# Kernel optimization log

Measured on AMD Instinct MI355X. Metric: run time of the kernel, lower is better.

The kernel has to match this reference:

```python
import jax, jax.numpy as jnp
import numpy as np

VOCAB = 50000
D = 256
NUM_GROUPS = 2
NUM_BEAMS = 4
MAX_LEN = 24
DIV_STRENGTH = 0.5


def setup_inputs() -> dict:
    key = jax.random.key(0)
    k1, k2, k3, k4 = jax.random.split(key, 4)
    B, S = 8, 128
    src = jax.random.normal(k1, (B, S, D), jnp.float32)
    We = jax.random.normal(k2, (D, D), jnp.float32) * (1.0 / np.sqrt(D))
    Emb = jax.random.normal(k3, (VOCAB, D), jnp.float32) * 0.02
    Wout = jax.random.normal(k4, (D, VOCAB), jnp.float32) * (1.0 / np.sqrt(D))
    return {"src": src, "We": We, "Emb": Emb, "Wout": Wout}


def _beam_search(src, We, Emb, Wout):
    B = src.shape[0]
    K, V, L = NUM_BEAMS, VOCAB, MAX_LEN

    # encoder: linear projection; decoder context = mean-pooled encoder output
    enc_out = jnp.einsum('bsd,de->bse', src, We)      # [B, S, D]
    ctx = enc_out.mean(axis=1)                        # [B, D]
    ctx_rep = jnp.repeat(ctx, K, axis=0)              # [B*K, D]
    beam_ids = jnp.arange(K)[:, None, None]           # [K,1,1]

    all_seqs, all_scores = [], []
    for g in range(NUM_GROUPS):
        prev = jnp.stack(all_seqs) if g > 0 else None  # [g, B, K, L]

        def step(carry, t, prev=prev):
            seqs, gs = carry                           # [B,K,L] int32, [B,K] f32
            tok = jax.lax.dynamic_index_in_dim(seqs, t - 1, axis=2, keepdims=False)  # [B,K]
            h = Emb[tok.reshape(-1)] + ctx_rep         # [B*K, D]
            logits = h @ Wout                          # [B*K, V]
            scores = jax.nn.log_softmax(logits, axis=-1).reshape(B, K, V)
            if prev is not None:
                # diversity penalty: subtract strength once per token present
                # anywhere (any batch, pos < t) in prev group's beam b (unique() semantics)
                posmask = (jnp.arange(L) < t).astype(scores.dtype)   # [L]
                w = jnp.broadcast_to(posmask, (K, B, L))

                def presence(pseq):                    # pseq: [B,K,L]
                    tok_t = pseq.transpose(1, 0, 2)    # [K,B,L]
                    cnt = jnp.zeros((K, V), scores.dtype).at[beam_ids, tok_t].add(w)
                    return (cnt > 0).astype(scores.dtype)

                pen = jax.vmap(presence)(prev).sum(axis=0)           # [K,V]
                scores = scores - DIV_STRENGTH * pen[None, :, :]
            total = (gs[:, :, None] + scores).reshape(B, K * V)
            topk_scores, topk_idx = jax.lax.top_k(total, K)          # [B,K]
            beam_idx = topk_idx // V
            next_tok = topk_idx % V
            seqs = jnp.take_along_axis(seqs, beam_idx[:, :, None], axis=1)
            seqs = seqs.at[:, :, t].set(next_tok)
            return (seqs, topk_scores), None

        init_scores = jnp.full((B, K), -1e9, jnp.float32).at[:, 0].set(0.0)
        init_seqs = jnp.zeros((B, K, L), jnp.int32).at[:, :, 0].set(1)  # BOS=1
        (seqs, gscores), _ = jax.lax.scan(step, (init_seqs, init_scores), jnp.arange(1, L))
        all_seqs.append(seqs)
        all_scores.append(gscores)

    return jnp.concatenate(all_seqs, axis=1), jnp.concatenate(all_scores, axis=1)


def reference(src, We, Emb, Wout):
    # returns (final_sequences [B, G*K, L] int32, final_scores [B, G*K] f32)
    return _beam_search(src, We, Emb, Wout)
```

## Files before the change

### kernel.cpp

```cpp
#include <hip/hip_runtime.h>
#include <math.h>

#define VOCAB 50000
#define DM 256
#define NB 8
#define NK 4
#define SL 24
#define NROW 32
#define CBLK 256
#define NXB 196
#define NPART NXB
#define DIVS 0.5f
#define NCH 49
#define SCH 1024

__device__ __forceinline__ bool cbetter(float av, int ai, float bv, int bi) {
  return (av > bv) || (av == bv && ai < bi);
}

__device__ __forceinline__ void merge4(const float* av, const int* ai,
                                       const float* bv, const int* bi,
                                       float* rv, int* ri) {
  int x = 0, y = 0;
#pragma unroll
  for (int j = 0; j < 4; ++j) {
    bool ta = cbetter(av[x], ai[x], bv[y], bi[y]);
    rv[j] = ta ? av[x] : bv[y];
    ri[j] = ta ? ai[x] : bi[y];
    if (ta) ++x; else ++y;
  }
}

__global__ void k_prep(const float* __restrict__ src, const float* __restrict__ We,
                       float* __restrict__ ctx) {
  int b = blockIdx.x, d = threadIdx.x;
  __shared__ float sm[DM];
  const float* p = src + (size_t)b * 128 * DM + d;
  float s = 0.f;
  for (int i = 0; i < 128; ++i) s += p[i * DM];
  sm[d] = s * (1.f / 128.f);
  __syncthreads();
  float acc = 0.f;
  for (int dp = 0; dp < DM; ++dp) acc += sm[dp] * We[dp * DM + d];
  ctx[b * DM + d] = acc;
}

__global__ void k_eprep(const float* __restrict__ Emb, const float* __restrict__ ctx,
                        const int* __restrict__ seq, float* __restrict__ eg, int t) {
  int r = blockIdx.x, d = threadIdx.x;
  int tok = seq[r * SL + (t - 1)];
  eg[r * DM + d] = Emb[(size_t)tok * DM + d] + ctx[(r >> 2) * DM + d];
}

__global__ void k_wtile(const float* __restrict__ Wout, float* __restrict__ WT) {
  int b = blockIdx.x, d = blockIdx.y, c = threadIdx.x;
  int col = b * CBLK + c;
  WT[(size_t)b * (CBLK * DM) + d * CBLK + c] =
      (col < VOCAB) ? Wout[(size_t)d * VOCAB + col] : 0.f;
}

__global__ __launch_bounds__(512) void k_logits_tiled(
    const float* __restrict__ WT, const float* __restrict__ eg,
    float* __restrict__ logits, float* __restrict__ pm, float* __restrict__ ps) {
  int tid = threadIdx.x;
  int lane = tid & 63, wq = tid >> 6;
  int c0 = blockIdx.x * CBLK + lane * 4;
  bool valid = (c0 + 3 < VOCAB);
  const float* wbase = WT + (size_t)blockIdx.x * (CBLK * DM) + lane * 4;
  int rb = __builtin_amdgcn_readfirstlane(wq) * 4;
  const float* e0 = eg + (size_t)rb * DM;
  float acc[4][4];
#pragma unroll
  for (int r = 0; r < 4; ++r)
#pragma unroll
    for (int c = 0; c < 4; ++c) acc[r][c] = 0.f;

  for (int d = 0; d < DM; d += 8) {
    float4 w[8];
#pragma unroll
    for (int j = 0; j < 8; ++j)
      w[j] = *reinterpret_cast<const float4*>(wbase + (size_t)(d + j) * CBLK);
#pragma unroll
    for (int r = 0; r < 4; ++r) {
      const float* ep = e0 + r * DM + d;
      const float4 ea = *reinterpret_cast<const float4*>(ep);
      const float4 eb = *reinterpret_cast<const float4*>(ep + 4);
#pragma unroll
      for (int c = 0; c < 4; ++c) {
        float a = acc[r][c];
        a = fmaf(ea.x, (&w[0].x)[c], a);
        a = fmaf(ea.y, (&w[1].x)[c], a);
        a = fmaf(ea.z, (&w[2].x)[c], a);
        a = fmaf(ea.w, (&w[3].x)[c], a);
        a = fmaf(eb.x, (&w[4].x)[c], a);
        a = fmaf(eb.y, (&w[5].x)[c], a);
        a = fmaf(eb.z, (&w[6].x)[c], a);
        a = fmaf(eb.w, (&w[7].x)[c], a);
        acc[r][c] = a;
      }
    }
  }
  if (valid) {
#pragma unroll
    for (int r = 0; r < 4; ++r) {
      float4 o = make_float4(acc[r][0], acc[r][1], acc[r][2], acc[r][3]);
      *reinterpret_cast<float4*>(&logits[(size_t)(rb + r) * VOCAB + c0]) = o;
    }
  }
#pragma unroll
  for (int r = 0; r < 4; ++r) {
    float m = valid ? fmaxf(fmaxf(acc[r][0], acc[r][1]), fmaxf(acc[r][2], acc[r][3]))
                    : -INFINITY;
#pragma unroll
    for (int o = 32; o >= 1; o >>= 1) m = fmaxf(m, __shfl_xor(m, o));
    float sv = 0.f;
    if (valid && m != -INFINITY) {
      sv = expf(acc[r][0] - m) + expf(acc[r][1] - m) +
           expf(acc[r][2] - m) + expf(acc[r][3] - m);
    }
#pragma unroll
    for (int o = 32; o >= 1; o >>= 1) sv += __shfl_xor(sv, o);
    if (lane == 0) {
      pm[(size_t)(rb + r) * NPART + blockIdx.x] = m;
      ps[(size_t)(rb + r) * NPART + blockIdx.x] = sv;
    }
  }
}

__global__ __launch_bounds__(512) void k_logits_flat(
    const float* __restrict__ Wout, const float* __restrict__ eg,
    float* __restrict__ logits, float* __restrict__ pm, float* __restrict__ ps) {
  int tid = threadIdx.x;
  int lane = tid & 63, wq = tid >> 6;
  int c0 = blockIdx.x * CBLK + lane * 4;
  bool valid = (c0 + 3 < VOCAB);
  const float* wbase = Wout + (valid ? c0 : (VOCAB - 4));
  int rb = __builtin_amdgcn_readfirstlane(wq) * 4;
  const float* e0 = eg + (size_t)rb * DM;
  float acc[4][4];
#pragma unroll
  for (int r = 0; r < 4; ++r)
#pragma unroll
    for (int c = 0; c < 4; ++c) acc[r][c] = 0.f;
  for (int d = 0; d < DM; d += 8) {
    float4 w[8];
#pragma unroll
    for (int j = 0; j < 8; ++j)
      w[j] = *reinterpret_cast<const float4*>(wbase + (size_t)(d + j) * VOCAB);
#pragma unroll
    for (int r = 0; r < 4; ++r) {
      const float* ep = e0 + r * DM + d;
      const float4 ea = *reinterpret_cast<const float4*>(ep);
      const float4 eb = *reinterpret_cast<const float4*>(ep + 4);
#pragma unroll
      for (int c = 0; c < 4; ++c) {
        float a = acc[r][c];
        a = fmaf(ea.x, (&w[0].x)[c], a);
        a = fmaf(ea.y, (&w[1].x)[c], a);
        a = fmaf(ea.z, (&w[2].x)[c], a);
        a = fmaf(ea.w, (&w[3].x)[c], a);
        a = fmaf(eb.x, (&w[4].x)[c], a);
        a = fmaf(eb.y, (&w[5].x)[c], a);
        a = fmaf(eb.z, (&w[6].x)[c], a);
        a = fmaf(eb.w, (&w[7].x)[c], a);
        acc[r][c] = a;
      }
    }
  }
  if (valid) {
#pragma unroll
    for (int r = 0; r < 4; ++r) {
      float4 o = make_float4(acc[r][0], acc[r][1], acc[r][2], acc[r][3]);
      *reinterpret_cast<float4*>(&logits[(size_t)(rb + r) * VOCAB + c0]) = o;
    }
  }
#pragma unroll
  for (int r = 0; r < 4; ++r) {
    float m = valid ? fmaxf(fmaxf(acc[r][0], acc[r][1]), fmaxf(acc[r][2], acc[r][3]))
                    : -INFINITY;
#pragma unroll
    for (int o = 32; o >= 1; o >>= 1) m = fmaxf(m, __shfl_xor(m, o));
    float sv = 0.f;
    if (valid && m != -INFINITY) {
      sv = expf(acc[r][0] - m) + expf(acc[r][1] - m) +
           expf(acc[r][2] - m) + expf(acc[r][3] - m);
    }
#pragma unroll
    for (int o = 32; o >= 1; o >>= 1) sv += __shfl_xor(sv, o);
    if (lane == 0) {
      pm[(size_t)(rb + r) * NPART + blockIdx.x] = m;
      ps[(size_t)(rb + r) * NPART + blockIdx.x] = sv;
    }
  }
}

__global__ __launch_bounds__(256) void k_topk_s1(
    const float* __restrict__ logits, const float* __restrict__ pm,
    const float* __restrict__ ps, const float* __restrict__ gs_src,
    const int* __restrict__ minpos, float* __restrict__ s1v,
    int* __restrict__ s1i, int t, int g) {
  int b = blockIdx.x / NCH, c = blockIdx.x % NCH, tid = threadIdx.x;
  int lane = tid & 63, wave = tid >> 6;
  __shared__ float gsv[NK], lsev[NK];
  __shared__ float lv[256][4];
  __shared__ int li[256][4];
  if (tid < NK) gsv[tid] = gs_src[b * NK + tid];
  {
    int row = b * NK + wave;
    const float* pmr = pm + (size_t)row * NPART;
    const float* psr = ps + (size_t)row * NPART;
    float M = -INFINITY, S = 0.f;
    for (int j = lane; j < NPART; j += 64) {
      float mj = pmr[j];
      if (mj != -INFINITY) {
        float sj = psr[j];
        float Mn = fmaxf(M, mj);
        S = (M == -INFINITY) ? sj * expf(mj - Mn)
                             : S * expf(M - Mn) + sj * expf(mj - Mn);
        M = Mn;
      }
    }
#pragma unroll
    for (int o = 32; o >= 1; o >>= 1) {
      float Mo = __shfl_xor(M, o);
      float So = __shfl_xor(S, o);
      if (Mo != -INFINITY) {
        float Mn = fmaxf(M, Mo);
        S = (M == -INFINITY) ? So * expf(Mo - Mn)
                             : S * expf(M - Mn) + So * expf(Mo - Mn);
        M = Mn;
      }
    }
    if (lane == 0) lsev[wave] = M + logf(S);
  }
  __syncthreads();

  float tv[4]; int ti[4];
#pragma unroll
  for (int j = 0; j < 4; ++j) { tv[j] = -INFINITY; ti[j] = 0x7fffffff; }

  int v = c * SCH + tid * 4;
  for (int k = 0; k < NK; ++k) {
    float gsk = gsv[k], lsek = lsev[k];
    const float* lrow = logits + (size_t)(b * NK + k) * VOCAB;
    const int* mp = minpos + (size_t)k * VOCAB;
    if (v + 3 < VOCAB) {
      float4 x4 = *reinterpret_cast<const float4*>(lrow + v);
      float xs[4] = {x4.x, x4.y, x4.z, x4.w};
      int pen[4] = {0, 0, 0, 0};
      if (g) {
        int4 m4 = *reinterpret_cast<const int4*>(mp + v);
        pen[0] = m4.x < t; pen[1] = m4.y < t; pen[2] = m4.z < t; pen[3] = m4.w < t;
      }
#pragma unroll
      for (int i = 0; i < 4; ++i) {
        float sc = xs[i] - lsek;
        if (pen[i]) sc -= DIVS;
        float x = gsk + sc;
        int idx = k * VOCAB + v + i;
        if (cbetter(x, idx, tv[3], ti[3])) {
          int pos = 3;
          if (cbetter(x, idx, tv[2], ti[2])) { tv[3]=tv[2]; ti[3]=ti[2]; pos=2;
            if (cbetter(x, idx, tv[1], ti[1])) { tv[2]=tv[1]; ti[2]=ti[1]; pos=1;
              if (cbetter(x, idx, tv[0], ti[0])) { tv[1]=tv[0]; ti[1]=ti[0]; pos=0; } } }
          tv[pos] = x; ti[pos] = idx;
        }
      }
    } else {
#pragma unroll
      for (int i = 0; i < 4; ++i) {
        int vv = v + i;
        if (vv >= VOCAB) break;
        float sc = lrow[vv] - lsek;
        if (g && mp[vv] < t) sc -= DIVS;
        float x = gsk + sc;
        int idx = k * VOCAB + vv;
        if (cbetter(x, idx, tv[3], ti[3])) {
          int pos = 3;
          if (cbetter(x, idx, tv[2], ti[2])) { tv[3]=tv[2]; ti[3]=ti[2]; pos=2;
            if (cbetter(x, idx, tv[1], ti[1])) { tv[2]=tv[1]; ti[2]=ti[1]; pos=1;
              if (cbetter(x, idx, tv[0], ti[0])) { tv[1]=tv[0]; ti[1]=ti[0]; pos=0; } } }
          tv[pos] = x; ti[pos] = idx;
        }
      }
    }
  }
#pragma unroll
  for (int j = 0; j < 4; ++j) { lv[tid][j] = tv[j]; li[tid][j] = ti[j]; }
  __syncthreads();
  for (int s = 128; s >= 1; s >>= 1) {
    if (tid < s) {
      float av[4], bv[4], rv[4]; int ai[4], bi[4], ri[4];
#pragma unroll
      for (int j = 0; j < 4; ++j) { av[j]=lv[tid][j]; ai[j]=li[tid][j]; bv[j]=lv[tid+s][j]; bi[j]=li[tid+s][j]; }
      merge4(av, ai, bv, bi, rv, ri);
#pragma unroll
      for (int j = 0; j < 4; ++j) { lv[tid][j]=rv[j]; li[tid][j]=ri[j]; }
    }
    __syncthreads();
  }
  if (tid == 0) {
#pragma unroll
    for (int j = 0; j < 4; ++j) {
      s1v[(b * NCH + c) * 4 + j] = lv[0][j];
      s1i[(b * NCH + c) * 4 + j] = li[0][j];
    }
  }
}

__global__ __launch_bounds__(256) void k_topk_s2(
    const float* __restrict__ s1v, const int* __restrict__ s1i,
    const int* __restrict__ seq_src, const float* __restrict__ Emb,
    const float* __restrict__ ctx, float* __restrict__ gs_dst,
    int* __restrict__ seq_dst, float* __restrict__ eg,
    int t, int g, float* __restrict__ out) {
  int b = blockIdx.x, tid = threadIdx.x;
  __shared__ float lv[64][4];
  __shared__ int li[64][4];
  __shared__ int oldseq[NK * SL];
  __shared__ float selv[NK];
  __shared__ int selb[NK], selt[NK];
  if (tid < 64) {
#pragma unroll
    for (int j = 0; j < 4; ++j) {
      if (tid < NCH) { lv[tid][j] = s1v[(b * NCH + tid) * 4 + j]; li[tid][j] = s1i[(b * NCH + tid) * 4 + j]; }
      else { lv[tid][j] = -INFINITY; li[tid][j] = 0x7fffffff; }
    }
  }
  if (tid < NK * SL) oldseq[tid] = seq_src[b * NK * SL + tid];
  __syncthreads();
  for (int s = 32; s >= 1; s >>= 1) {
    if (tid < s) {
      float av[4], bv[4], rv[4]; int ai[4], bi[4], ri[4];
#pragma unroll
      for (int j = 0; j < 4; ++j) { av[j]=lv[tid][j]; ai[j]=li[tid][j]; bv[j]=lv[tid+s][j]; bi[j]=li[tid+s][j]; }
      merge4(av, ai, bv, bi, rv, ri);
#pragma unroll
      for (int j = 0; j < 4; ++j) { lv[tid][j]=rv[j]; li[tid][j]=ri[j]; }
    }
    __syncthreads();
  }
  if (tid == 0) {
#pragma unroll
    for (int j = 0; j < 4; ++j) {
      selv[j] = lv[0][j];
      selb[j] = li[0][j] / VOCAB;
      selt[j] = li[0][j] % VOCAB;
    }
  }
  __syncthreads();
  if (tid < NK * SL) {
    int j = tid / SL, l = tid % SL;
    int tok = (l == t) ? selt[j] : oldseq[selb[j] * SL + l];
    seq_dst[b * NK * SL + tid] = tok;
    if (t == SL - 1) out[(size_t)b * (2 * NK * SL) + (g * NK + j) * SL + l] = (float)tok;
  }
  if (tid < NK) {
    gs_dst[b * NK + tid] = selv[tid];
    if (t == SL - 1) out[NB * 2 * NK * SL + b * (2 * NK) + g * NK + tid] = selv[tid];
  }
  if (t < SL - 1) {
    int d = tid;
#pragma unroll
    for (int j = 0; j < NK; ++j) {
      int nt_ = selt[j];
      eg[(size_t)(b * NK + j) * DM + d] = Emb[(size_t)nt_ * DM + d] + ctx[b * DM + d];
    }
  }
}

__global__ void k_init(int* __restrict__ seqA, float* __restrict__ gsA) {
  int i = threadIdx.x;
  seqA[i] = (i % SL == 0) ? 1 : 0;
  if (i < NB * NK) gsA[i] = ((i & 3) == 0) ? 0.f : -1e9f;
}

__global__ void k_minpos_init(int* __restrict__ minpos) {
  int i = blockIdx.x * 256 + threadIdx.x;
  if (i < NK * VOCAB) minpos[i] = 1 << 30;
}

__global__ void k_minpos_scatter(const int* __restrict__ seq, int* __restrict__ minpos) {
  int i = threadIdx.x;
  int l = i % SL;
  int k = (i / SL) % NK;
  int tok = seq[i];
  atomicMin(&minpos[(size_t)k * VOCAB + tok], l);
}

extern "C" void kernel_launch(void* const* d_in, const int* in_sizes, int n_in,
                              void* d_out, int out_size, void* d_ws, size_t ws_size,
                              hipStream_t stream) {
  (void)in_sizes; (void)n_in; (void)out_size;
  const float* src  = (const float*)d_in[0];
  const float* We   = (const float*)d_in[1];
  const float* Emb  = (const float*)d_in[2];
  const float* Wout = (const float*)d_in[3];
  float* out = (float*)d_out;
  char* ws = (char*)d_ws;
  size_t off = 0;
  auto carve = [&](size_t bytes) {
    char* p = ws + off;
    off += (bytes + 255) & ~(size_t)255;
    return p;
  };
  float* ctx    = (float*)carve((size_t)NB * DM * 4);
  float* eg     = (float*)carve((size_t)NROW * DM * 4);
  float* logits = (float*)carve((size_t)NROW * VOCAB * 4);
  float* pm     = (float*)carve((size_t)NROW * NPART * 4);
  float* ps     = (float*)carve((size_t)NROW * NPART * 4);
  int*   seqA   = (int*)carve((size_t)NB * NK * SL * 4);
  int*   seqB   = (int*)carve((size_t)NB * NK * SL * 4);
  float* gsA    = (float*)carve((size_t)NROW * 4);
  float* gsB    = (float*)carve((size_t)NROW * 4);
  int*   minpos = (int*)carve((size_t)NK * VOCAB * 4);
  float* s1v    = (float*)carve((size_t)NB * NCH * 4 * 4);
  int*   s1i    = (int*)carve((size_t)NB * NCH * 4 * 4);
  size_t wt_bytes = (size_t)NXB * CBLK * DM * 4;
  bool use_tile = (off + wt_bytes + 256 <= ws_size);
  float* WT = use_tile ? (float*)carve(wt_bytes) : nullptr;

  hipLaunchKernelGGL(k_prep, dim3(NB), dim3(DM), 0, stream, src, We, ctx);
  if (use_tile)
    hipLaunchKernelGGL(k_wtile, dim3(NXB, DM), dim3(CBLK), 0, stream, Wout, WT);

  for (int g = 0; g < 2; ++g) {
    hipLaunchKernelGGL(k_init, dim3(1), dim3(768), 0, stream, seqA, gsA);
    for (int t = 1; t < SL; ++t) {
      int* ssrc = ((t - 1) & 1) ? seqB : seqA;
      int* sdst = (t & 1) ? seqB : seqA;
      float* gsrc = ((t - 1) & 1) ? gsB : gsA;
      float* gdst = (t & 1) ? gsB : gsA;
      if (t == 1)
        hipLaunchKernelGGL(k_eprep, dim3(NROW), dim3(DM), 0, stream,
                           Emb, ctx, ssrc, eg, t);
      if (use_tile)
        hipLaunchKernelGGL(k_logits_tiled, dim3(NXB), dim3(512), 0, stream,
                           WT, eg, logits, pm, ps);
      else
        hipLaunchKernelGGL(k_logits_flat, dim3(NXB), dim3(512), 0, stream,
                           Wout, eg, logits, pm, ps);
      hipLaunchKernelGGL(k_topk_s1, dim3(NB * NCH), dim3(256), 0, stream,
                         logits, pm, ps, gsrc, minpos, s1v, s1i, t, g);
      hipLaunchKernelGGL(k_topk_s2, dim3(NB), dim3(256), 0, stream,
                         s1v, s1i, ssrc, Emb, ctx, gdst, sdst, eg, t, g, out);
    }
    if (g == 0) {
      hipLaunchKernelGGL(k_minpos_init, dim3((NK * VOCAB + 255) / 256), dim3(256), 0, stream, minpos);
      hipLaunchKernelGGL(k_minpos_scatter, dim3(1), dim3(768), 0, stream, seqB, minpos);
    }
  }
}
```

Before: 2.247 ms.

## Split top-k stage one per beam row and defer softmax normalization to stage two

Stage one of the top-k now runs one block per (batch, beam, chunk) on raw penalized logits, with no logsumexp work, and packs a penalty flag into the candidate index. Stage two now does the partial-max/sum combine for the logsumexp. It then rescales the per-row candidates with beam score, normalizer and penalty, and selects the final top-4 over all rows. This removes the per-block redundant logsumexp reduction and the serial loop over four beams, giving four times more blocks to spread across the GPU. The cost is more stage-one blocks writing more candidates, and a heavier single-block-per-batch stage two.

Result: slower. 2.512 ms (+11.8%).

```diff
diff --git a/kernel.cpp b/kernel.cpp
--- a/kernel.cpp
+++ b/kernel.cpp
@@ -13,6 +13,7 @@
 #define DIVS 0.5f
 #define NCH 49
 #define SCH 1024
+#define CINV 0x7fffffff
 
 __device__ __forceinline__ bool cbetter(float av, int ai, float bv, int bi) {
   return (av > bv) || (av == bv && ai < bi);
@@ -25,6 +26,19 @@
 #pragma unroll
   for (int j = 0; j < 4; ++j) {
     bool ta = cbetter(av[x], ai[x], bv[y], bi[y]);
+    rv[j] = ta ? av[x] : bv[y];
+    ri[j] = ta ? ai[x] : bi[y];
+    if (ta) ++x; else ++y;
+  }
+}
+
+__device__ __forceinline__ void merge4c(const float* av, const int* ai,
+                                        const float* bv, const int* bi,
+                                        float* rv, int* ri) {
+  int x = 0, y = 0;
+#pragma unroll
+  for (int j = 0; j < 4; ++j) {
+    bool ta = cbetter(av[x], ai[x] & 0xFFFF, bv[y], bi[y] & 0xFFFF);
     rv[j] = ta ? av[x] : bv[y];
     ri[j] = ta ? ai[x] : bi[y];
     if (ta) ++x; else ++y;
@@ -195,16 +209,103 @@
 }
 
 __global__ __launch_bounds__(256) void k_topk_s1(
-    const float* __restrict__ logits, const float* __restrict__ pm,
-    const float* __restrict__ ps, const float* __restrict__ gs_src,
-    const int* __restrict__ minpos, float* __restrict__ s1v,
-    int* __restrict__ s1i, int t, int g) {
-  int b = blockIdx.x / NCH, c = blockIdx.x % NCH, tid = threadIdx.x;
+    const float* __restrict__ logits, const int* __restrict__ minpos,
+    float* __restrict__ s1v, int* __restrict__ s1i, int t, int g) {
+  int blk = blockIdx.x;
+  int b = blk / (NK * NCH);
+  int k = (blk / NCH) % NK;
+  int c = blk % NCH;
+  int tid = threadIdx.x;
+  __shared__ float lv[256][4];
+  __shared__ int li[256][4];
+
+  const float* lrow = logits + (size_t)(b * NK + k) * VOCAB;
+  const int* mp = minpos + (size_t)k * VOCAB;
+
+  float tv[4]; int ti[4];
+#pragma unroll
+  for (int j = 0; j < 4; ++j) { tv[j] = -INFINITY; ti[j] = CINV; }
+
+  int v = c * SCH + tid * 4;
+  if (v + 3 < VOCAB) {
+    float4 x4 = *reinterpret_cast<const float4*>(lrow + v);
+    float xs[4] = {x4.x, x4.y, x4.z, x4.w};
+    int pen[4] = {0, 0, 0, 0};
+    if (g) {
+      int4 m4 = *reinterpret_cast<const int4*>(mp + v);
+      pen[0] = m4.x < t; pen[1] = m4.y < t; pen[2] = m4.z < t; pen[3] = m4.w < t;
+    }
+#pragma unroll
+    for (int i = 0; i < 4; ++i) {
+      float key = xs[i] - (pen[i] ? 0.5f : 0.0f);
+      int col = v + i;
+      int vp = col | (pen[i] << 16);
+      if (cbetter(key, col, tv[3], ti[3] & 0xFFFF)) {
+        int pos = 3;
+        if (cbetter(key, col, tv[2], ti[2] & 0xFFFF)) { tv[3]=tv[2]; ti[3]=ti[2]; pos=2;
+          if (cbetter(key, col, tv[1], ti[1] & 0xFFFF)) { tv[2]=tv[1]; ti[2]=ti[1]; pos=1;
+            if (cbetter(key, col, tv[0], ti[0] & 0xFFFF)) { tv[1]=tv[0]; ti[1]=ti[0]; pos=0; } } }
+        tv[pos] = key; ti[pos] = vp;
+      }
+    }
+  } else {
+#pragma unroll
+    for (int i = 0; i < 4; ++i) {
+      int vv = v + i;
+      if (vv >= VOCAB) break;
+      int pen = (g && mp[vv] < t) ? 1 : 0;
+      float key = lrow[vv] - (pen ? 0.5f : 0.0f);
+      int vp = vv | (pen << 16);
+      if (cbetter(key, vv, tv[3], ti[3] & 0xFFFF)) {
+        int pos = 3;
+        if (cbetter(key, vv, tv[2], ti[2] & 0xFFFF)) { tv[3]=tv[2]; ti[3]=ti[2]; pos=2;
+          if (cbetter(key, vv, tv[1], ti[1] & 0xFFFF)) { tv[2]=tv[1]; ti[2]=ti[1]; pos=1;
+            if (cbetter(key, vv, tv[0], ti[0] & 0xFFFF)) { tv[1]=tv[0]; ti[1]=ti[0]; pos=0; } } }
+        tv[pos] = key; ti[pos] = vp;
+      }
+    }
+  }
+#pragma unroll
+  for (int j = 0; j < 4; ++j) { lv[tid][j] = tv[j]; li[tid][j] = ti[j]; }
+  __syncthreads();
+  for (int s = 128; s >= 1; s >>= 1) {
+    if (tid < s) {
+      float av[4], bv[4], rv[4]; int ai[4], bi[4], ri[4];
+#pragma unroll
+      for (int j = 0; j < 4; ++j) { av[j]=lv[tid][j]; ai[j]=li[tid][j]; bv[j]=lv[tid+s][j]; bi[j]=li[tid+s][j]; }
+      merge4c(av, ai, bv, bi, rv, ri);
+#pragma unroll
+      for (int j = 0; j < 4; ++j) { lv[tid][j]=rv[j]; li[tid][j]=ri[j]; }
+    }
+    __syncthreads();
+  }
+  if (tid == 0) {
+    size_t base = ((size_t)(b * NK + k) * NCH + c) * 4;
+#pragma unroll
+    for (int j = 0; j < 4; ++j) {
+      s1v[base + j] = lv[0][j];
+      s1i[base + j] = li[0][j];
+    }
+  }
+}
+
+__global__ __launch_bounds__(256) void k_topk_s2(
+    const float* __restrict__ s1v, const int* __restrict__ s1i,
+    const float* __restrict__ pm, const float* __restrict__ ps,
+    const float* __restrict__ gs_src, const int* __restrict__ seq_src,
+    const float* __restrict__ Emb, const float* __restrict__ ctx,
+    float* __restrict__ gs_dst, int* __restrict__ seq_dst,
+    float* __restrict__ eg, int t, int g, float* __restrict__ out) {
+  int b = blockIdx.x, tid = threadIdx.x;
   int lane = tid & 63, wave = tid >> 6;
   __shared__ float gsv[NK], lsev[NK];
   __shared__ float lv[256][4];
   __shared__ int li[256][4];
+  __shared__ int oldseq[NK * SL];
+  __shared__ float selv[NK];
+  __shared__ int selb[NK], selt[NK];
   if (tid < NK) gsv[tid] = gs_src[b * NK + tid];
+  if (tid < NK * SL) oldseq[tid] = seq_src[b * NK * SL + tid];
   {
     int row = b * NK + wave;
     const float* pmr = pm + (size_t)row * NPART;
@@ -237,99 +338,33 @@
 
   float tv[4]; int ti[4];
 #pragma unroll
-  for (int j = 0; j < 4; ++j) { tv[j] = -INFINITY; ti[j] = 0x7fffffff; }
-
-  int v = c * SCH + tid * 4;
-  for (int k = 0; k < NK; ++k) {
-    float gsk = gsv[k], lsek = lsev[k];
-    const float* lrow = logits + (size_t)(b * NK + k) * VOCAB;
-    const int* mp = minpos + (size_t)k * VOCAB;
-    if (v + 3 < VOCAB) {
-      float4 x4 = *reinterpret_cast<const float4*>(lrow + v);
-      float xs[4] = {x4.x, x4.y, x4.z, x4.w};
-      int pen[4] = {0, 0, 0, 0};
-      if (g) {
-        int4 m4 = *reinterpret_cast<const int4*>(mp + v);
-        pen[0] = m4.x < t; pen[1] = m4.y < t; pen[2] = m4.z < t; pen[3] = m4.w < t;
-      }
-#pragma unroll
-      for (int i = 0; i < 4; ++i) {
-        float sc = xs[i] - lsek;
-        if (pen[i]) sc -= DIVS;
-        float x = gsk + sc;
-        int idx = k * VOCAB + v + i;
-        if (cbetter(x, idx, tv[3], ti[3])) {
-          int pos = 3;
-          if (cbetter(x, idx, tv[2], ti[2])) { tv[3]=tv[2]; ti[3]=ti[2]; pos=2;
-            if (cbetter(x, idx, tv[1], ti[1])) { tv[2]=tv[1]; ti[2]=ti[1]; pos=1;
-              if (cbetter(x, idx, tv[0], ti[0])) { tv[1]=tv[0]; ti[1]=ti[0]; pos=0; } } }
-          tv[pos] = x; ti[pos] = idx;
-        }
-      }
-    } else {
-#pragma unroll
-      for (int i = 0; i < 4; ++i) {
-        int vv = v + i;
-        if (vv >= VOCAB) break;
-        float sc = lrow[vv] - lsek;
-        if (g && mp[vv] < t) sc -= DIVS;
-        float x = gsk + sc;
-        int idx = k * VOCAB + vv;
-        if (cbetter(x, idx, tv[3], ti[3])) {
-          int pos = 3;
-          if (cbetter(x, idx, tv[2], ti[2])) { tv[3]=tv[2]; ti[3]=ti[2]; pos=2;
-            if (cbetter(x, idx, tv[1], ti[1])) { tv[2]=tv[1]; ti[2]=ti[1]; pos=1;
-              if (cbetter(x, idx, tv[0], ti[0])) { tv[1]=tv[0]; ti[1]=ti[0]; pos=0; } } }
-          tv[pos] = x; ti[pos] = idx;
-        }
-      }
+  for (int j = 0; j < 4; ++j) { tv[j] = -INFINITY; ti[j] = CINV; }
+  const int PERROW = NCH * 4;
+  for (int cc = tid; cc < NK * PERROW; cc += 256) {
+    int r = cc / PERROW, e = cc - r * PERROW;
+    size_t addr = (size_t)(b * NK + r) * PERROW + e;
+    float key = s1v[addr];
+    int vp = s1i[addr];
+    if (vp == CINV) continue;
+    int pen = (vp >> 16) & 1;
+    int col = vp & 0xFFFF;
+    float l = key + (pen ? 0.5f : 0.0f);
+    float sc = l - lsev[r];
+    if (pen) sc -= DIVS;
+    float x = gsv[r] + sc;
+    int idx = r * VOCAB + col;
+    if (cbetter(x, idx, tv[3], ti[3])) {
+      int pos = 3;
+      if (cbetter(x, idx, tv[2], ti[2])) { tv[3]=tv[2]; ti[3]=ti[2]; pos=2;
+        if (cbetter(x, idx, tv[1], ti[1])) { tv[2]=tv[1]; ti[2]=ti[1]; pos=1;
+          if (cbetter(x, idx, tv[0], ti[0])) { tv[1]=tv[0]; ti[1]=ti[0]; pos=0; } } }
+      tv[pos] = x; ti[pos] = idx;
     }
   }
 #pragma unroll
   for (int j = 0; j < 4; ++j) { lv[tid][j] = tv[j]; li[tid][j] = ti[j]; }
   __syncthreads();
   for (int s = 128; s >= 1; s >>= 1) {
-    if (tid < s) {
-      float av[4], bv[4], rv[4]; int ai[4], bi[4], ri[4];
-#pragma unroll
-      for (int j = 0; j < 4; ++j) { av[j]=lv[tid][j]; ai[j]=li[tid][j]; bv[j]=lv[tid+s][j]; bi[j]=li[tid+s][j]; }
-      merge4(av, ai, bv, bi, rv, ri);
-#pragma unroll
-      for (int j = 0; j < 4; ++j) { lv[tid][j]=rv[j]; li[tid][j]=ri[j]; }
-    }
-    __syncthreads();
-  }
-  if (tid == 0) {
-#pragma unroll
-    for (int j = 0; j < 4; ++j) {
-      s1v[(b * NCH + c) * 4 + j] = lv[0][j];
-      s1i[(b * NCH + c) * 4 + j] = li[0][j];
-    }
-  }
-}
-
-__global__ __launch_bounds__(256) void k_topk_s2(
-    const float* __restrict__ s1v, const int* __restrict__ s1i,
-    const int* __restrict__ seq_src, const float* __restrict__ Emb,
-    const float* __restrict__ ctx, float* __restrict__ gs_dst,
-    int* __restrict__ seq_dst, float* __restrict__ eg,
-    int t, int g, float* __restrict__ out) {
-  int b = blockIdx.x, tid = threadIdx.x;
-  __shared__ float lv[64][4];
-  __shared__ int li[64][4];
-  __shared__ int oldseq[NK * SL];
-  __shared__ float selv[NK];
-  __shared__ int selb[NK], selt[NK];
-  if (tid < 64) {
-#pragma unroll
-    for (int j = 0; j < 4; ++j) {
-      if (tid < NCH) { lv[tid][j] = s1v[(b * NCH + tid) * 4 + j]; li[tid][j] = s1i[(b * NCH + tid) * 4 + j]; }
-      else { lv[tid][j] = -INFINITY; li[tid][j] = 0x7fffffff; }
-    }
-  }
-  if (tid < NK * SL) oldseq[tid] = seq_src[b * NK * SL + tid];
-  __syncthreads();
-  for (int s = 32; s >= 1; s >>= 1) {
     if (tid < s) {
       float av[4], bv[4], rv[4]; int ai[4], bi[4], ri[4];
 #pragma unroll
@@ -414,8 +449,8 @@
   float* gsA    = (float*)carve((size_t)NROW * 4);
   float* gsB    = (float*)carve((size_t)NROW * 4);
   int*   minpos = (int*)carve((size_t)NK * VOCAB * 4);
-  float* s1v    = (float*)carve((size_t)NB * NCH * 4 * 4);
-  int*   s1i    = (int*)carve((size_t)NB * NCH * 4 * 4);
+  float* s1v    = (float*)carve((size_t)NB * NK * NCH * 4 * 4);
+  int*   s1i    = (int*)carve((size_t)NB * NK * NCH * 4 * 4);
   size_t wt_bytes = (size_t)NXB * CBLK * DM * 4;
   bool use_tile = (off + wt_bytes + 256 <= ws_size);
   float* WT = use_tile ? (float*)carve(wt_bytes) : nullptr;
@@ -440,10 +475,11 @@
       else
         hipLaunchKernelGGL(k_logits_flat, dim3(NXB), dim3(512), 0, stream,
                            Wout, eg, logits, pm, ps);
-      hipLaunchKernelGGL(k_topk_s1, dim3(NB * NCH), dim3(256), 0, stream,
-                         logits, pm, ps, gsrc, minpos, s1v, s1i, t, g);
+      hipLaunchKernelGGL(k_topk_s1, dim3(NB * NK * NCH), dim3(256), 0, stream,
+                         logits, minpos, s1v, s1i, t, g);
       hipLaunchKernelGGL(k_topk_s2, dim3(NB), dim3(256), 0, stream,
-                         s1v, s1i, ssrc, Emb, ctx, gdst, sdst, eg, t, g, out);
+                         s1v, s1i, pm, ps, gsrc, ssrc, Emb, ctx,
+                         gdst, sdst, eg, t, g, out);
     }
     if (g == 0) {
       hipLaunchKernelGGL(k_minpos_init, dim3((NK * VOCAB + 255) / 256), dim3(256), 0, stream, minpos);
```
